# Kernel tuning notes

Measured on AMD Instinct MI355X. Metric: run time of the kernel, lower is better.

## Reference

```python
import jax, jax.numpy as jnp
import numpy as np

H = 1024  # hidden_size
IN = 1    # input_size
OUT = 1   # out_size


def _lstm_cell(x, h, c, W_ih, W_hh, b_ih, b_hh):
    # PyTorch LSTMCell: gates ordered (i, f, g, o)
    gates = x @ W_ih.T + h @ W_hh.T + (b_ih + b_hh)
    i, f, g, o = jnp.split(gates, 4, axis=-1)
    c_new = jax.nn.sigmoid(f) * c + jax.nn.sigmoid(i) * jnp.tanh(g)
    h_new = jax.nn.sigmoid(o) * jnp.tanh(c_new)
    return h_new, c_new


def setup_inputs() -> dict:
    key = jax.random.key(0)
    ks = jax.random.split(key, 12)
    B, T = 128, 256
    s1 = 1.0 / np.sqrt(H)
    u = lambda k, shp: jax.random.uniform(k, shp, jnp.float32, -s1, s1)
    return {
        "x": jax.random.normal(ks[0], (B, T), jnp.float32),
        "W_ih1": u(ks[1], (4 * H, IN)),
        "W_hh1": u(ks[2], (4 * H, H)),
        "b_ih1": u(ks[3], (4 * H,)),
        "b_hh1": u(ks[4], (4 * H,)),
        "W_ih2": u(ks[5], (4 * H, H)),
        "W_hh2": u(ks[6], (4 * H, H)),
        "b_ih2": u(ks[7], (4 * H,)),
        "b_hh2": u(ks[8], (4 * H,)),
        "W_lin": u(ks[9], (OUT, H)),
        "b_lin": u(ks[10], (OUT,)),
        "future": 64,
    }


def reference(x, W_ih1, W_hh1, b_ih1, b_hh1, W_ih2, W_hh2, b_ih2, b_hh2,
              W_lin, b_lin, future):
    B = x.shape[0]
    z = jnp.zeros((B, H), x.dtype)
    carry0 = (z, z, z, z)
    xs = jnp.swapaxes(x, 0, 1)[:, :, None]  # [T, B, 1]

    def cell_stack(carry, inp):
        h1, c1, h2, c2 = carry
        h1, c1 = _lstm_cell(inp, h1, c1, W_ih1, W_hh1, b_ih1, b_hh1)
        h2, c2 = _lstm_cell(h1, h2, c2, W_ih2, W_hh2, b_ih2, b_hh2)
        out = h2 @ W_lin.T + b_lin  # [B, 1]
        return (h1, c1, h2, c2), out

    carry, outs = jax.lax.scan(cell_stack, carry0, xs)  # outs: [T, B, 1]

    if future > 0:
        def ar_step(carry, _):
            h1, c1, h2, c2, out = carry
            (h1, c1, h2, c2), new_out = cell_stack((h1, c1, h2, c2), out)
            return (h1, c1, h2, c2, new_out), new_out

        _, outs2 = jax.lax.scan(ar_step, (*carry, outs[-1]), None, length=future)
        outs = jnp.concatenate([outs, outs2], axis=0)

    return jnp.swapaxes(outs[..., 0], 0, 1)  # [B, T+future]
```

## Files before the change

### kernel.cpp

```cpp
#include <hip/hip_runtime.h>


typedef _Float16 f16;
typedef _Float16 f16x8 __attribute__((ext_vector_type(8)));
typedef _Float16 f16x4 __attribute__((ext_vector_type(4)));
typedef float    f32x4 __attribute__((ext_vector_type(4)));
typedef int      i32x4 __attribute__((ext_vector_type(4)));
typedef unsigned int   u32;

#define NB   256
#define WGS  512
#define HS   1024
#define BS   128
#define TS   256
#define TTS  320
#define KST  32
#define PSTR 131072
#define NT   3

#define OFF_H1    0u
#define OFF_H2    524288u
#define OFF_CNT1  1048576u
#define OFF_CNT2  1179648u
#define OFF_FLAG  1310720u
#define OFF_XREG  1376256u
#define OFF_ACC8  1376768u
#define WS_END    2687488u

#define NSLOT       64
#define SLOT_TGT    4
#define SLOT_STRIDE 512

#define LDS_G1    98304
#define LDS_G2    106496
#define LDS_XF    114688
#define LDS_PRM   115200
#define LDS_MISC  115456
#define LDS_SH1   115584
#define LDS_SH2   116608
#define LDS_TOTAL 117760

__device__ __forceinline__ float sigm(float x){ return 1.0f/(1.0f + __expf(-x)); }

__device__ __forceinline__ void wt_store(u32* p, u32 v) {
  __hip_atomic_store(p, v, __ATOMIC_RELAXED, __HIP_MEMORY_SCOPE_AGENT);
}

__device__ __forceinline__ void st16_wt(f16* addr, f16x8 v) {
  i32x4 d = __builtin_bit_cast(i32x4, v);
  asm volatile("global_store_dwordx4 %0, %1, off sc0 sc1"
               :: "v"(addr), "v"(d) : "memory");
}

__device__ __forceinline__ void poll_slots(const int* cnt, int t) {
  const int* p = cnt + (threadIdx.x & 63) * SLOT_STRIDE + t;
  while (__hip_atomic_load(p, __ATOMIC_RELAXED, __HIP_MEMORY_SCOPE_AGENT) < SLOT_TGT)
    __builtin_amdgcn_s_sleep(1);
}

__global__ void init_ws_kernel(char* ws){
  const size_t n = (WS_END - OFF_CNT1) / 16u;
  float4* r = (float4*)(ws + OFF_CNT1);
  float4 z = make_float4(0.f, 0.f, 0.f, 0.f);
  size_t stride = (size_t)gridDim.x * blockDim.x;
  for (size_t i = blockIdx.x*(size_t)blockDim.x + threadIdx.x; i < n; i += stride) r[i] = z;
  __builtin_amdgcn_fence(__ATOMIC_RELEASE, "agent");
}

__global__ void __launch_bounds__(WGS, 2)
lstm_coop(const float* __restrict__ xg,
          const float* __restrict__ Wih1, const float* __restrict__ Whh1,
          const float* __restrict__ bih1, const float* __restrict__ bhh1,
          const float* __restrict__ Wih2, const float* __restrict__ Whh2,
          const float* __restrict__ bih2, const float* __restrict__ bhh2,
          const float* __restrict__ Wlin, const float* __restrict__ blin,
          float* __restrict__ outp, char* __restrict__ ws)
{
  extern __shared__ char smem[];
  f16*   Wlds = (f16*)smem;
  float* g1s  = (float*)(smem + LDS_G1);
  float* g2s  = (float*)(smem + LDS_G2);
  float* xfd  = (float*)(smem + LDS_XF);
  float* prm  = (float*)(smem + LDS_PRM);
  int*   miscl= (int*)(smem + LDS_MISC);
  f16*   sh1  = (f16*)(smem + LDS_SH1);
  f16*   sh2  = (f16*)(smem + LDS_SH2);

  f16* H1  = (f16*)(ws + OFF_H1);
  f16* H2  = (f16*)(ws + OFF_H2);
  int* cnt1 = (int*)(ws + OFF_CNT1);
  int* cnt2 = (int*)(ws + OFF_CNT2);
  int* flags= (int*)(ws + OFF_FLAG);
  float* accs8 = (float*)(ws + OFF_ACC8);

  const int tid = threadIdx.x;
  const int blk = blockIdx.x;

  int xcd_raw;
  asm("s_getreg_b32 %0, hwreg(HW_REG_XCC_ID)" : "=s"(xcd_raw));
  if (tid == 0) {
    int x = xcd_raw & 7;
    int rank = __hip_atomic_fetch_add((int*)(ws + OFF_XREG) + x*16, 1,
                                      __ATOMIC_RELAXED, __HIP_MEMORY_SCOPE_AGENT);
    miscl[0] = x;
    miscl[1] = (rank == 0) ? 1 : 0;
  }

  for (int item = tid; item < NT*KST*64; item += WGS) {
    int tile = item >> 11;
    int rem  = item & 2047;
    int k0   = rem >> 6;
    int lane = rem & 63;
    int n    = lane & 15;
    int kbase = k0*32 + (lane>>4)*8;
    const float* Wsrc = (tile==0) ? Whh1 : (tile==1) ? Wih2 : Whh2;
    const float* p = Wsrc + (size_t)((n>>2)*1024 + blk*4 + (n&3))*HS + kbase;
    f16x8 pk;
    #pragma unroll
    for (int j=0;j<8;j++) pk[j] = (f16)p[j];
    *(f16x8*)(Wlds + (size_t)item*8) = pk;
  }
  if (tid < 16) {
    int row = (tid>>2)*1024 + blk*4 + (tid&3);
    prm[tid]      = Wih1[row];
    prm[16 + tid] = bih1[row] + bhh1[row];
    prm[32 + tid] = bih2[row] + bhh2[row];
  }
  if (tid == 16) prm[48] = blin[0];

  const int erow = tid >> 2;
  const int eu   = tid & 3;
  const float wlin_c = Wlin[blk*4 + eu];
  float c1 = 0.f, c2 = 0.f;
  __syncthreads();

  const int  myxcd  = miscl[0];
  const bool leader = miscl[1] != 0;
  int* flag = flags + myxcd * 2048;
  float* myacc = accs8 + (size_t)myxcd * TTS * BS;

  const int wv    = tid >> 6;
  const int lane  = tid & 63;
  const int n15   = lane & 15;
  const int mrow  = wv*16 + n15;
  const int kc    = (lane>>4)*8;
  const int rbase = wv*16 + (lane>>4)*4;
  const f16x8* WB = (const f16x8*)Wlds;
  const int abase = mrow*4 + (kc>>2)*512;

  for (int t = 0; t < TTS; ++t) {
    const int p1 = t & 1;
    const int p2 = (t + 1) & 1;

    if (t >= TS) {
      if (wv == 7) poll_slots(cnt2, t);
      __syncthreads();
      if (tid < BS) {
        float s = 0.f;
        #pragma unroll
        for (int x = 0; x < 8; ++x)
          s += __hip_atomic_load(accs8 + ((size_t)x*TTS + (t-1))*BS + tid,
                                 __ATOMIC_RELAXED, __HIP_MEMORY_SCOPE_AGENT);
        xfd[tid] = s + prm[48];
      }
      __syncthreads();
    }

    {
      float h1v;
      if (t == 0) {
        float xv = xg[erow*TS + 0];
        float gi = xv*prm[0*4+eu] + prm[16 + 0*4+eu];
        float gg = xv*prm[2*4+eu] + prm[16 + 2*4+eu];
        float go = xv*prm[3*4+eu] + prm[16 + 3*4+eu];
        c1 = sigm(gi)*tanhf(gg);
        h1v = sigm(go)*tanhf(c1);
      } else {
        float xv = (t < TS) ? xg[erow*TS + t] : xfd[erow];
        float gi = g1s[erow*16 + 0*4+eu] + xv*prm[0*4+eu];
        float gf = g1s[erow*16 + 1*4+eu] + xv*prm[1*4+eu];
        float gg = g1s[erow*16 + 2*4+eu] + xv*prm[2*4+eu];
        float go = g1s[erow*16 + 3*4+eu] + xv*prm[3*4+eu];
        c1 = sigm(gf)*c1 + sigm(gi)*tanhf(gg);
        h1v = sigm(go)*tanhf(c1);
      }
      sh1[tid] = (f16)h1v;
    }
    __syncthreads();

    if (wv == 0) {
      st16_wt(H1 + (size_t)p1*PSTR + blk*512 + lane*8, *(const f16x8*)(sh1 + lane*8));
      asm volatile("s_waitcnt vmcnt(0)" ::: "memory");
      if (lane == 0)
        __hip_atomic_fetch_add(cnt1 + (blk & (NSLOT-1))*SLOT_STRIDE + t, 1,
                               __ATOMIC_RELAXED, __HIP_MEMORY_SCOPE_AGENT);
    }

    if (wv == 7) {
      if (leader) {
        if (t >= 1) poll_slots(cnt2, t);
        poll_slots(cnt1, t);
        __builtin_amdgcn_fence(__ATOMIC_ACQUIRE, "agent");
        asm volatile("s_waitcnt vmcnt(0)" ::: "memory");
        if (lane == 0)
          __hip_atomic_store(flag, t + 1, __ATOMIC_RELAXED, __HIP_MEMORY_SCOPE_AGENT);
      } else {
        if (lane == 0) {
          while (__hip_atomic_load(flag, __ATOMIC_RELAXED, __HIP_MEMORY_SCOPE_AGENT) < t + 1)
            __builtin_amdgcn_s_sleep(1);
        }
      }
    }
    __syncthreads();

    if (t >= 1 && blk == ((t-1) & 255) && tid < BS) {
      float v;
      if (t >= TS) {
        v = xfd[tid];
      } else {
        float s = 0.f;
        #pragma unroll
        for (int x = 0; x < 8; ++x)
          s += __hip_atomic_load(accs8 + ((size_t)x*TTS + (t-1))*BS + tid,
                                 __ATOMIC_RELAXED, __HIP_MEMORY_SCOPE_AGENT);
        v = s + prm[48];
      }
      wt_store((u32*)&outp[tid*TTS + (t-1)], __builtin_bit_cast(u32, v));
    }

    const f16* A1 = H1 + (size_t)p1*PSTR + abase;
    const f16* A2 = H2 + (size_t)p2*PSTR + abase;
    f32x4 acc1  = {0.f,0.f,0.f,0.f};
    f32x4 acc2a = {0.f,0.f,0.f,0.f};
    f32x4 acc2b = {0.f,0.f,0.f,0.f};
    if (t == 0) {
      #pragma unroll 8
      for (int k0 = 0; k0 < KST; ++k0) {
        f16x4 a1l = *(const f16x4*)(A1 + k0*4096);
        f16x4 a1h = *(const f16x4*)(A1 + k0*4096 + 512);
        f16x8 a1  = __builtin_shufflevector(a1l, a1h, 0,1,2,3,4,5,6,7);
        f16x8 b0 = WB[(0*KST + k0)*64 + lane];
        f16x8 b1 = WB[(1*KST + k0)*64 + lane];
        acc1  = __builtin_amdgcn_mfma_f32_16x16x32_f16(a1, b0, acc1,  0,0,0);
        acc2a = __builtin_amdgcn_mfma_f32_16x16x32_f16(a1, b1, acc2a, 0,0,0);
      }
    } else {
      #pragma unroll 8
      for (int k0 = 0; k0 < KST; ++k0) {
        f16x4 a1l = *(const f16x4*)(A1 + k0*4096);
        f16x4 a1h = *(const f16x4*)(A1 + k0*4096 + 512);
        f16x4 a2l = *(const f16x4*)(A2 + k0*4096);
        f16x4 a2h = *(const f16x4*)(A2 + k0*4096 + 512);
        f16x8 a1  = __builtin_shufflevector(a1l, a1h, 0,1,2,3,4,5,6,7);
        f16x8 a2  = __builtin_shufflevector(a2l, a2h, 0,1,2,3,4,5,6,7);
        f16x8 b0 = WB[(0*KST + k0)*64 + lane];
        f16x8 b1 = WB[(1*KST + k0)*64 + lane];
        f16x8 b2 = WB[(2*KST + k0)*64 + lane];
        acc1  = __builtin_amdgcn_mfma_f32_16x16x32_f16(a1, b0, acc1,  0,0,0);
        acc2a = __builtin_amdgcn_mfma_f32_16x16x32_f16(a1, b1, acc2a, 0,0,0);
        acc2b = __builtin_amdgcn_mfma_f32_16x16x32_f16(a2, b2, acc2b, 0,0,0);
      }
    }
    #pragma unroll
    for (int r = 0; r < 4; ++r) {
      int grow = rbase + r;
      g1s[grow*16 + n15] = acc1[r]  + prm[16 + n15];
      g2s[grow*16 + n15] = acc2a[r] + acc2b[r] + prm[32 + n15];
    }
    __syncthreads();

    {
      float gi = g2s[erow*16 + 0*4+eu];
      float gf = g2s[erow*16 + 1*4+eu];
      float gg = g2s[erow*16 + 2*4+eu];
      float go = g2s[erow*16 + 3*4+eu];
      c2 = sigm(gf)*c2 + sigm(gi)*tanhf(gg);
      float h2v = sigm(go)*tanhf(c2);
      sh2[tid] = (f16)h2v;
      float p = h2v * wlin_c;
      p += __shfl_xor(p, 1);
      p += __shfl_xor(p, 2);
      if (eu == 0)
        __hip_atomic_fetch_add(myacc + (size_t)t*BS + erow, p,
                               __ATOMIC_RELAXED, __HIP_MEMORY_SCOPE_AGENT);
    }

    asm volatile("s_waitcnt vmcnt(0)" ::: "memory");
    __syncthreads();

    if (wv == 1) {
      st16_wt(H2 + (size_t)p1*PSTR + blk*512 + lane*8, *(const f16x8*)(sh2 + lane*8));
      asm volatile("s_waitcnt vmcnt(0)" ::: "memory");
      if (lane == 0)
        __hip_atomic_fetch_add(cnt2 + (blk & (NSLOT-1))*SLOT_STRIDE + (t+1), 1,
                               __ATOMIC_RELAXED, __HIP_MEMORY_SCOPE_AGENT);
    }
  }

  if (blk == 63) {
    if (wv == 7) poll_slots(cnt2, TTS);
    __syncthreads();
    if (tid < BS) {
      float s = 0.f;
      #pragma unroll
      for (int x = 0; x < 8; ++x)
        s += __hip_atomic_load(accs8 + ((size_t)x*TTS + (TTS-1))*BS + tid,
                               __ATOMIC_RELAXED, __HIP_MEMORY_SCOPE_AGENT);
      wt_store((u32*)&outp[tid*TTS + (TTS-1)],
               __builtin_bit_cast(u32, s + prm[48]));
    }
  }
}

extern "C" void kernel_launch(void* const* d_in, const int* in_sizes, int n_in,
                              void* d_out, int out_size, void* d_ws, size_t ws_size,
                              hipStream_t stream) {
  const float* xg   = (const float*)d_in[0];
  const float* Wih1 = (const float*)d_in[1];
  const float* Whh1 = (const float*)d_in[2];
  const float* bih1 = (const float*)d_in[3];
  const float* bhh1 = (const float*)d_in[4];
  const float* Wih2 = (const float*)d_in[5];
  const float* Whh2 = (const float*)d_in[6];
  const float* bih2 = (const float*)d_in[7];
  const float* bhh2 = (const float*)d_in[8];
  const float* Wlin = (const float*)d_in[9];
  const float* blin = (const float*)d_in[10];
  float* outp = (float*)d_out;
  char* ws = (char*)d_ws;

  init_ws_kernel<<<dim3(128), dim3(256), 0, stream>>>(ws);

  (void)hipFuncSetAttribute((const void*)lstm_coop,
                            hipFuncAttributeMaxDynamicSharedMemorySize, LDS_TOTAL);

  void* args[] = { (void*)&xg, (void*)&Wih1, (void*)&Whh1, (void*)&bih1, (void*)&bhh1,
                   (void*)&Wih2, (void*)&Whh2, (void*)&bih2, (void*)&bhh2,
                   (void*)&Wlin, (void*)&blin, (void*)&outp, (void*)&ws };
  hipError_t err = hipLaunchCooperativeKernel((const void*)lstm_coop,
                                              dim3(NB), dim3(WGS), args, LDS_TOTAL, stream);
  if (err != hipSuccess) {
    lstm_coop<<<dim3(NB), dim3(WGS), LDS_TOTAL, stream>>>(
        xg, Wih1, Whh1, bih1, bhh1, Wih2, Whh2, bih2, bhh2, Wlin, blin, outp, ws);
  }
}
```

Measured before the change: 4.634 ms.

## Compute next-step layer-1 state at end of iteration during teacher-forced phase

Result: faster. 4.516 ms (-2.5%).

```diff
diff --git a/kernel.cpp b/kernel.cpp
--- a/kernel.cpp
+++ b/kernel.cpp
@@ -148,6 +148,24 @@
   const f16x8* WB = (const f16x8*)Wlds;
   const int abase = mrow*4 + (kc>>2)*512;
 
+  {
+    float xv = xg[erow*TS + 0];
+    float gi = xv*prm[0*4+eu] + prm[16 + 0*4+eu];
+    float gg = xv*prm[2*4+eu] + prm[16 + 2*4+eu];
+    float go = xv*prm[3*4+eu] + prm[16 + 3*4+eu];
+    c1 = sigm(gi)*tanhf(gg);
+    float h1v = sigm(go)*tanhf(c1);
+    sh1[tid] = (f16)h1v;
+  }
+  __syncthreads();
+  if (wv == 0) {
+    st16_wt(H1 + (size_t)0*PSTR + blk*512 + lane*8, *(const f16x8*)(sh1 + lane*8));
+    asm volatile("s_waitcnt vmcnt(0)" ::: "memory");
+    if (lane == 0)
+      __hip_atomic_fetch_add(cnt1 + (blk & (NSLOT-1))*SLOT_STRIDE + 0, 1,
+                             __ATOMIC_RELAXED, __HIP_MEMORY_SCOPE_AGENT);
+  }
+
   for (int t = 0; t < TTS; ++t) {
     const int p1 = t & 1;
     const int p2 = (t + 1) & 1;
@@ -164,36 +182,24 @@
         xfd[tid] = s + prm[48];
       }
       __syncthreads();
-    }
-
-    {
-      float h1v;
-      if (t == 0) {
-        float xv = xg[erow*TS + 0];
-        float gi = xv*prm[0*4+eu] + prm[16 + 0*4+eu];
-        float gg = xv*prm[2*4+eu] + prm[16 + 2*4+eu];
-        float go = xv*prm[3*4+eu] + prm[16 + 3*4+eu];
-        c1 = sigm(gi)*tanhf(gg);
-        h1v = sigm(go)*tanhf(c1);
-      } else {
-        float xv = (t < TS) ? xg[erow*TS + t] : xfd[erow];
+      {
+        float xv = xfd[erow];
         float gi = g1s[erow*16 + 0*4+eu] + xv*prm[0*4+eu];
         float gf = g1s[erow*16 + 1*4+eu] + xv*prm[1*4+eu];
         float gg = g1s[erow*16 + 2*4+eu] + xv*prm[2*4+eu];
         float go = g1s[erow*16 + 3*4+eu] + xv*prm[3*4+eu];
         c1 = sigm(gf)*c1 + sigm(gi)*tanhf(gg);
-        h1v = sigm(go)*tanhf(c1);
-      }
-      sh1[tid] = (f16)h1v;
-    }
-    __syncthreads();
-
-    if (wv == 0) {
-      st16_wt(H1 + (size_t)p1*PSTR + blk*512 + lane*8, *(const f16x8*)(sh1 + lane*8));
-      asm volatile("s_waitcnt vmcnt(0)" ::: "memory");
-      if (lane == 0)
-        __hip_atomic_fetch_add(cnt1 + (blk & (NSLOT-1))*SLOT_STRIDE + t, 1,
-                               __ATOMIC_RELAXED, __HIP_MEMORY_SCOPE_AGENT);
+        float h1v = sigm(go)*tanhf(c1);
+        sh1[tid] = (f16)h1v;
+      }
+      __syncthreads();
+      if (wv == 0) {
+        st16_wt(H1 + (size_t)p1*PSTR + blk*512 + lane*8, *(const f16x8*)(sh1 + lane*8));
+        asm volatile("s_waitcnt vmcnt(0)" ::: "memory");
+        if (lane == 0)
+          __hip_atomic_fetch_add(cnt1 + (blk & (NSLOT-1))*SLOT_STRIDE + t, 1,
+                                 __ATOMIC_RELAXED, __HIP_MEMORY_SCOPE_AGENT);
+      }
     }
 
     if (wv == 7) {
@@ -213,20 +219,8 @@
     }
     __syncthreads();
 
-    if (t >= 1 && blk == ((t-1) & 255) && tid < BS) {
-      float v;
-      if (t >= TS) {
-        v = xfd[tid];
-      } else {
-        float s = 0.f;
-        #pragma unroll
-        for (int x = 0; x < 8; ++x)
-          s += __hip_atomic_load(accs8 + ((size_t)x*TTS + (t-1))*BS + tid,
-                                 __ATOMIC_RELAXED, __HIP_MEMORY_SCOPE_AGENT);
-        v = s + prm[48];
-      }
-      wt_store((u32*)&outp[tid*TTS + (t-1)], __builtin_bit_cast(u32, v));
-    }
+    float xv_next = 0.0f;
+    if (t + 1 <= TS-1) xv_next = xg[erow*TS + (t+1)];
 
     const f16* A1 = H1 + (size_t)p1*PSTR + abase;
     const f16* A2 = H2 + (size_t)p2*PSTR + abase;
@@ -285,15 +279,48 @@
                                __ATOMIC_RELAXED, __HIP_MEMORY_SCOPE_AGENT);
     }
 
+    if (t + 1 <= TS-1) {
+      float xv = xv_next;
+      float gi = g1s[erow*16 + 0*4+eu] + xv*prm[0*4+eu];
+      float gf = g1s[erow*16 + 1*4+eu] + xv*prm[1*4+eu];
+      float gg = g1s[erow*16 + 2*4+eu] + xv*prm[2*4+eu];
+      float go = g1s[erow*16 + 3*4+eu] + xv*prm[3*4+eu];
+      c1 = sigm(gf)*c1 + sigm(gi)*tanhf(gg);
+      float h1v = sigm(go)*tanhf(c1);
+      sh1[tid] = (f16)h1v;
+    }
+
     asm volatile("s_waitcnt vmcnt(0)" ::: "memory");
     __syncthreads();
 
+    if (wv == 0 && t + 1 <= TS-1) {
+      st16_wt(H1 + (size_t)p2*PSTR + blk*512 + lane*8, *(const f16x8*)(sh1 + lane*8));
+      asm volatile("s_waitcnt vmcnt(0)" ::: "memory");
+      if (lane == 0)
+        __hip_atomic_fetch_add(cnt1 + (blk & (NSLOT-1))*SLOT_STRIDE + (t+1), 1,
+                               __ATOMIC_RELAXED, __HIP_MEMORY_SCOPE_AGENT);
+    }
     if (wv == 1) {
       st16_wt(H2 + (size_t)p1*PSTR + blk*512 + lane*8, *(const f16x8*)(sh2 + lane*8));
       asm volatile("s_waitcnt vmcnt(0)" ::: "memory");
       if (lane == 0)
         __hip_atomic_fetch_add(cnt2 + (blk & (NSLOT-1))*SLOT_STRIDE + (t+1), 1,
                                __ATOMIC_RELAXED, __HIP_MEMORY_SCOPE_AGENT);
+    }
+
+    if (t >= 1 && blk == ((t-1) & 255) && tid < BS) {
+      float v;
+      if (t >= TS) {
+        v = xfd[tid];
+      } else {
+        float s = 0.f;
+        #pragma unroll
+        for (int x = 0; x < 8; ++x)
+          s += __hip_atomic_load(accs8 + ((size_t)x*TTS + (t-1))*BS + tid,
+                                 __ATOMIC_RELAXED, __HIP_MEMORY_SCOPE_AGENT);
+        v = s + prm[48];
+      }
+      wt_store((u32*)&outp[tid*TTS + (t-1)], __builtin_bit_cast(u32, v));
     }
   }
 
```
